# Optimization experiments

Measured on AMD Instinct MI355X. Metric: run time of the kernel, lower is better.

The kernel has to match this reference:

```python
import jax, jax.numpy as jnp
import numpy as np

B, CQ, CKV, H, W = 4, 128, 256, 64, 64
NUM_HEADS = 8
SCALE = (CQ // NUM_HEADS) ** (-0.5)


def setup_inputs() -> dict:
    key = jax.random.key(0)
    ks = jax.random.split(key, 10)
    s = 0.02
    return {
        "x_q": jax.random.normal(ks[0], (B, CQ, H, W), dtype=jnp.float32),
        "x_kv": jax.random.normal(ks[1], (B, CKV, H, W), dtype=jnp.float32),
        "Wq": jax.random.normal(ks[2], (CQ, CQ), dtype=jnp.float32) * s,
        "bq": jnp.zeros((CQ,), dtype=jnp.float32),
        "Wk": jax.random.normal(ks[3], (CQ, CKV), dtype=jnp.float32) * s,
        "bk": jnp.zeros((CQ,), dtype=jnp.float32),
        "Wv": jax.random.normal(ks[4], (CQ, CKV), dtype=jnp.float32) * s,
        "bv": jnp.zeros((CQ,), dtype=jnp.float32),
        "Wo": jax.random.normal(ks[5], (CQ, CQ), dtype=jnp.float32) * s,
        "bo": jnp.zeros((CQ,), dtype=jnp.float32),
    }


def _conv1x1(x, Wm, bv_):
    # 1x1 conv == channel-mixing matmul: [B,C,H,W] x [O,C] -> [B,O,H,W]
    return jnp.einsum('bchw,oc->bohw', x, Wm) + bv_[:, None, None]


def reference(x_q, x_kv, Wq, bq, Wk, bk, Wv, bv, Wo, bo):
    b, c, h, w = x_q.shape
    n = h * w
    Q = _conv1x1(x_q, Wq, bq).reshape(b, c, n)   # [B,C,N]
    K = _conv1x1(x_kv, Wk, bk).reshape(b, c, n)  # [B,C,N]
    V = _conv1x1(x_kv, Wv, bv).reshape(b, c, n)  # [B,C,N]
    # attn = softmax(Q^T K * scale) over keys: [B,N,N]
    attn = jax.nn.softmax(jnp.einsum('bcn,bcm->bnm', Q, K) * SCALE, axis=-1)
    out = jnp.einsum('bnm,bcm->bcn', attn, V).reshape(b, c, h, w)
    out = _conv1x1(out, Wo, bo) + x_q
    return out
```

## Files before the change

### kernel.cpp

```cpp
#include <hip/hip_runtime.h>
#include <hip/hip_bf16.h>

typedef __bf16 bf16x8 __attribute__((ext_vector_type(8)));
typedef float f32x4 __attribute__((ext_vector_type(4)));
typedef float f32x16 __attribute__((ext_vector_type(16)));

#define MFMA16(a, b, c) __builtin_amdgcn_mfma_f32_16x16x32_bf16(a, b, c, 0, 0, 0)
#define MFMA32(a, b, c) __builtin_amdgcn_mfma_f32_32x32x16_bf16(a, b, c, 0, 0, 0)

static constexpr int NSP = 4096;
static constexpr float SCALE_L2E = 0.25f * 1.4426950408889634f;

__device__ __forceinline__ bf16x8 ld_frag(const void* p) {
  int4 v = *(const int4*)p;
  return __builtin_bit_cast(bf16x8, v);
}

__device__ __forceinline__ unsigned pk2(float a, float b) {
  unsigned short x = __builtin_bit_cast(unsigned short, (__bf16)a);
  unsigned short y = __builtin_bit_cast(unsigned short, (__bf16)b);
  return (unsigned)x | ((unsigned)y << 16);
}

__device__ __forceinline__ void load_lds16(const void* g, void* l) {
  __builtin_amdgcn_global_load_lds(
      (const __attribute__((address_space(1))) unsigned*)g,
      (__attribute__((address_space(3))) unsigned*)l, 16, 0, 0);
}

__global__ void k_prep(const float* __restrict__ Wq, const float* __restrict__ bq,
                       const float* __restrict__ Wk, const float* __restrict__ Wv,
                       const float* __restrict__ Wo,
                       __bf16* __restrict__ wqb, __bf16* __restrict__ wkb,
                       __bf16* __restrict__ wvb, __bf16* __restrict__ wob,
                       float* __restrict__ bqs) {
  int i = blockIdx.x * 256 + threadIdx.x;
  if (i < 16384)      wqb[i]          = (__bf16)(Wq[i] * SCALE_L2E);
  else if (i < 49152) wkb[i - 16384]  = (__bf16)Wk[i - 16384];
  else if (i < 81920) wvb[i - 49152]  = (__bf16)Wv[i - 49152];
  else if (i < 98304) wob[i - 81920]  = (__bf16)Wo[i - 81920];
  if (i < 128) bqs[i] = bq[i] * SCALE_L2E;
}

template <bool SWZ>
__device__ __forceinline__ void store_tile_T(char* myt, const f32x4* acc, int g, int r,
                                             __bf16* dst_base) {
#pragma unroll
  for (int oc = 0; oc < 8; ++oc) {
#pragma unroll
    for (int rr = 0; rr < 4; ++rr) {
      int o = oc * 16 + g * 4 + rr;
      int byte = (r << 8) + (o << 1);
      byte ^= (r & 7) << 4;
      *(__bf16*)(myt + byte) = (__bf16)acc[oc][rr];
    }
  }
  int l = g * 16 + r;
#pragma unroll
  for (int p = 0; p < 4; ++p) {
    int u = p * 64 + l, row = u >> 4, seg = u & 15;
    int byte = (row << 8) + (seg << 4);
    if (!SWZ) byte ^= (row & 7) << 4;
    int4 v = *(int4*)(myt + byte);
    *(int4*)(dst_base + row * 128 + seg * 8) = v;
  }
}

__global__ __launch_bounds__(256) void k_proj(const float* __restrict__ xq,
                                              const float* __restrict__ xkv,
                                              const __bf16* __restrict__ wqb,
                                              const __bf16* __restrict__ wkb,
                                              const __bf16* __restrict__ wvb,
                                              const float* __restrict__ bqs,
                                              const float* __restrict__ bk,
                                              const float* __restrict__ bv,
                                              __bf16* __restrict__ Qt,
                                              __bf16* __restrict__ Kt,
                                              __bf16* __restrict__ Vm) {
  const int t = threadIdx.x, w = t >> 6, l = t & 63, r = l & 15, g = l >> 4;
  __shared__ __align__(16) char lds[16384];
  char* myt = lds + (w << 12);

  if (blockIdx.x < 256) {
    const int b = blockIdx.x >> 6;
    const int n0 = (blockIdx.x & 63) << 6;
    const int nl = n0 + (w << 4) + r;
    const float* xb = xq + ((size_t)b << 19);
    bf16x8 bx[4];
#pragma unroll
    for (int cc = 0; cc < 4; ++cc) {
#pragma unroll
      for (int i = 0; i < 8; ++i) {
        int c = cc * 32 + g * 8 + i;
        bx[cc][i] = (__bf16)xb[c * 4096 + nl];
      }
    }
    f32x4 acc[8];
#pragma unroll
    for (int oc = 0; oc < 8; ++oc)
#pragma unroll
      for (int rr = 0; rr < 4; ++rr) acc[oc][rr] = bqs[oc * 16 + g * 4 + rr];
#pragma unroll
    for (int oc = 0; oc < 8; ++oc) {
#pragma unroll
      for (int cc = 0; cc < 4; ++cc) {
        bf16x8 a = ld_frag(wqb + (oc * 16 + r) * 128 + cc * 32 + g * 8);
        acc[oc] = MFMA16(a, bx[cc], acc[oc]);
      }
    }
    store_tile_T<false>(myt, acc, g, r, Qt + ((size_t)(b * NSP + n0 + w * 16)) * 128);
  } else {
    const int bid = blockIdx.x - 256;
    const int b = bid >> 6;
    const int n0 = (bid & 63) << 6;
    const int nl = n0 + (w << 4) + r;
    const float* xb = xkv + ((size_t)b << 20);
    bf16x8 bx[8];
#pragma unroll
    for (int cc = 0; cc < 8; ++cc) {
#pragma unroll
      for (int i = 0; i < 8; ++i) {
        int c = cc * 32 + g * 8 + i;
        bx[cc][i] = (__bf16)xb[(size_t)c * 4096 + nl];
      }
    }
    f32x4 acc[8];
#pragma unroll
    for (int oc = 0; oc < 8; ++oc)
#pragma unroll
      for (int rr = 0; rr < 4; ++rr) acc[oc][rr] = bk[oc * 16 + g * 4 + rr];
#pragma unroll
    for (int oc = 0; oc < 8; ++oc) {
#pragma unroll
      for (int cc = 0; cc < 8; ++cc) {
        bf16x8 a = ld_frag(wkb + (oc * 16 + r) * 256 + cc * 32 + g * 8);
        acc[oc] = MFMA16(a, bx[cc], acc[oc]);
      }
    }
    store_tile_T<true>(myt, acc, g, r, Kt + ((size_t)(b * NSP + n0 + w * 16)) * 128);

    f32x4 av[8];
#pragma unroll
    for (int oc = 0; oc < 8; ++oc)
#pragma unroll
      for (int rr = 0; rr < 4; ++rr) av[oc][rr] = bv[oc * 16 + g * 4 + rr];
#pragma unroll
    for (int oc = 0; oc < 8; ++oc) {
#pragma unroll
      for (int cc = 0; cc < 8; ++cc) {
        bf16x8 a = ld_frag(wvb + (oc * 16 + r) * 256 + cc * 32 + g * 8);
        av[oc] = MFMA16(a, bx[cc], av[oc]);
      }
    }
#pragma unroll
    for (int oc = 0; oc < 8; ++oc) {
#pragma unroll
      for (int rr = 0; rr < 4; ++rr) {
        int o = oc * 16 + g * 4 + rr;
        Vm[((size_t)(b * 128 + o) << 12) + (nl ^ ((o & 7) << 3))] = (__bf16)av[oc][rr];
      }
    }
  }
}

template <int SPLIT>
__global__ __launch_bounds__(256, 2) void k_flash(const __bf16* __restrict__ Qt,
                                                  const __bf16* __restrict__ Kt,
                                                  const __bf16* __restrict__ Vm,
                                                  __bf16* __restrict__ Op,
                                                  float2* __restrict__ Ml) {
  const int bid = blockIdx.x;
  const int combo = bid & (4 * SPLIT - 1), qtile = bid / (4 * SPLIT);
  const int b = combo & 3, ks = combo >> 2;
  const int q0 = qtile << 7;
  const int NK = NSP / SPLIT;
  const int t = threadIdx.x, w = t >> 6, l = t & 63;
  const int q31 = l & 31, hi = l >> 5;
  const int swz = (q31 & 7) << 4;

  __shared__ __align__(16) char kl[2][16384];
  __shared__ __align__(16) char vl[2][16384];

  const __bf16* qp = Qt + ((size_t)(b * NSP + q0 + w * 32 + q31)) * 128;
  bf16x8 qf[8];
#pragma unroll
  for (int cc = 0; cc < 8; ++cc) qf[cc] = ld_frag(qp + cc * 16 + hi * 8);

  f32x16 acc[4];
#pragma unroll
  for (int c = 0; c < 4; ++c)
#pragma unroll
    for (int i = 0; i < 16; ++i) acc[c][i] = 0.f;
  float m = -1e30f, lsum = 0.f;

  const char* kbase = (const char*)(Kt + ((size_t)(b * NSP) + ks * NK) * 128);
  const char* vbase = (const char*)(Vm + (size_t)b * 128 * NSP + ks * NK);

  auto STAGE = [&](int bi, int tt) {
#pragma unroll
    for (int i = 0; i < 4; ++i) {
      int c = i * 4 + w;
      load_lds16(kbase + tt * 16384 + c * 1024 + l * 16, &kl[bi][c * 1024]);
    }
#pragma unroll
    for (int i = 0; i < 4; ++i) {
      int c0 = (i * 4 + w) * 8;
      int ch = c0 + (l >> 3);
      load_lds16(vbase + (size_t)ch * 8192 + tt * 128 + (l & 7) * 16,
                 &vl[bi][c0 * 128]);
    }
  };

  STAGE(0, 0);
  __syncthreads();

  const int nit = NK / 64;
  for (int it = 0; it < nit; ++it) {
    const int cur = it & 1;
    if (it + 1 < nit) STAGE(cur ^ 1, it + 1);

    const char* kt = kl[cur];
    f32x16 s0 = {}, s1 = {};
    __builtin_amdgcn_s_setprio(1);
#pragma unroll
    for (int cc = 0; cc < 8; ++cc) {
      int cb = (cc * 32 + hi * 16);
      int a0 = (q31 << 8) + (cb ^ swz);
      s0 = MFMA32(ld_frag(kt + a0), qf[cc], s0);
      int a1 = ((32 + q31) << 8) + (cb ^ swz);
      s1 = MFMA32(ld_frag(kt + a1), qf[cc], s1);
    }
    __builtin_amdgcn_s_setprio(0);

    float mx = s0[0];
#pragma unroll
    for (int i = 1; i < 16; ++i) mx = fmaxf(mx, s0[i]);
#pragma unroll
    for (int i = 0; i < 16; ++i) mx = fmaxf(mx, s1[i]);
    mx = fmaxf(mx, __shfl_xor(mx, 32));
    if (__any(mx - m > 8.f)) {
      float mn = fmaxf(m, mx);
      float a = exp2f(m - mn);
      m = mn;
      lsum *= a;
#pragma unroll
      for (int c = 0; c < 4; ++c)
#pragma unroll
        for (int i = 0; i < 16; ++i) acc[c][i] *= a;
    }
    float rs = 0.f;
#pragma unroll
    for (int i = 0; i < 16; ++i) {
      s0[i] = exp2f(s0[i] - m);
      rs += s0[i];
    }
#pragma unroll
    for (int i = 0; i < 16; ++i) {
      s1[i] = exp2f(s1[i] - m);
      rs += s1[i];
    }
    rs += __shfl_xor(rs, 32);
    lsum += rs;

    unsigned o0[4][2], o1[4][2], r0[4][2], r1[4][2];
#pragma unroll
    for (int q4 = 0; q4 < 4; ++q4) {
      o0[q4][0] = pk2(s0[4 * q4 + 0], s0[4 * q4 + 1]);
      o0[q4][1] = pk2(s0[4 * q4 + 2], s0[4 * q4 + 3]);
      o1[q4][0] = pk2(s1[4 * q4 + 0], s1[4 * q4 + 1]);
      o1[q4][1] = pk2(s1[4 * q4 + 2], s1[4 * q4 + 3]);
    }
#pragma unroll
    for (int q4 = 0; q4 < 4; ++q4) {
      r0[q4][0] = __shfl_xor(o0[q4][0], 32);
      r0[q4][1] = __shfl_xor(o0[q4][1], 32);
      r1[q4][0] = __shfl_xor(o1[q4][0], 32);
      r1[q4][1] = __shfl_xor(o1[q4][1], 32);
    }

    const char* vt = vl[cur];
    __builtin_amdgcn_s_setprio(1);
#pragma unroll
    for (int kb = 0; kb < 2; ++kb) {
      uint4 f0, f1;
      f0.x = hi ? r0[2 * kb + 1][0] : o0[2 * kb][0];
      f0.y = hi ? r0[2 * kb + 1][1] : o0[2 * kb][1];
      f0.z = hi ? o0[2 * kb + 1][0] : r0[2 * kb][0];
      f0.w = hi ? o0[2 * kb + 1][1] : r0[2 * kb][1];
      f1.x = hi ? r1[2 * kb + 1][0] : o1[2 * kb][0];
      f1.y = hi ? r1[2 * kb + 1][1] : o1[2 * kb][1];
      f1.z = hi ? o1[2 * kb + 1][0] : r1[2 * kb][0];
      f1.w = hi ? o1[2 * kb + 1][1] : r1[2 * kb][1];
      bf16x8 pf0 = __builtin_bit_cast(bf16x8, f0);
      bf16x8 pf1 = __builtin_bit_cast(bf16x8, f1);
#pragma unroll
      for (int cht = 0; cht < 4; ++cht) {
        int rowb = (cht * 32 + q31) << 7;
        int va0 = rowb + ((kb * 32 + hi * 16) ^ swz);
        acc[cht] = MFMA32(ld_frag(vt + va0), pf0, acc[cht]);
        int va1 = rowb + ((64 + kb * 32 + hi * 16) ^ swz);
        acc[cht] = MFMA32(ld_frag(vt + va1), pf1, acc[cht]);
      }
    }
    __builtin_amdgcn_s_setprio(0);
    __syncthreads();
  }

  float inv = 1.f / lsum;
  const size_t orow = (size_t)((ks * 4 + b) * NSP + q0 + w * 32 + q31) * 128;
#pragma unroll
  for (int cht = 0; cht < 4; ++cht) {
#pragma unroll
    for (int qq = 0; qq < 4; ++qq) {
      uint2 v;
      v.x = pk2(acc[cht][4 * qq + 0] * inv, acc[cht][4 * qq + 1] * inv);
      v.y = pk2(acc[cht][4 * qq + 2] * inv, acc[cht][4 * qq + 3] * inv);
      *(uint2*)(Op + orow + cht * 32 + qq * 8 + hi * 4) = v;
    }
  }
  if (hi == 0) {
    Ml[(size_t)(ks * 4 + b) * NSP + q0 + w * 32 + q31] = make_float2(m, lsum);
  }
}

template <int SPLIT>
__global__ __launch_bounds__(256) void k_oproj(const __bf16* __restrict__ Op,
                                               const float2* __restrict__ Ml,
                                               const __bf16* __restrict__ wob,
                                               const float* __restrict__ bo,
                                               const float* __restrict__ xq,
                                               float* __restrict__ out) {
  const int b = blockIdx.x >> 6;
  const int n0 = (blockIdx.x & 63) << 6;
  const int t = threadIdx.x, w = t >> 6, l = t & 63, r = l & 15, g = l >> 4;
  const int nl = n0 + (w << 4) + r;

  float2 e[SPLIT];
  float M = -1e30f;
#pragma unroll
  for (int s = 0; s < SPLIT; ++s) {
    e[s] = Ml[(size_t)(s * 4 + b) * NSP + nl];
    M = fmaxf(M, e[s].x);
  }
  float wk[SPLIT], den = 0.f;
#pragma unroll
  for (int s = 0; s < SPLIT; ++s) {
    wk[s] = exp2f(e[s].x - M);
    den += e[s].y * wk[s];
  }
  float inv = 1.f / den;
#pragma unroll
  for (int s = 0; s < SPLIT; ++s) wk[s] *= inv;

  bf16x8 bfr[4];
#pragma unroll
  for (int cc = 0; cc < 4; ++cc) {
    float a8[8];
#pragma unroll
    for (int j = 0; j < 8; ++j) a8[j] = 0.f;
#pragma unroll
    for (int s = 0; s < SPLIT; ++s) {
      bf16x8 a = ld_frag(Op + ((size_t)(s * 4 + b) * NSP + nl) * 128 + cc * 32 + g * 8);
#pragma unroll
      for (int j = 0; j < 8; ++j) a8[j] += (float)a[j] * wk[s];
    }
#pragma unroll
    for (int j = 0; j < 8; ++j) bfr[cc][j] = (__bf16)a8[j];
  }

  f32x4 acc[8];
#pragma unroll
  for (int oc = 0; oc < 8; ++oc)
#pragma unroll
    for (int rr = 0; rr < 4; ++rr) acc[oc][rr] = bo[oc * 16 + g * 4 + rr];
#pragma unroll
  for (int oc = 0; oc < 8; ++oc) {
#pragma unroll
    for (int cc = 0; cc < 4; ++cc) {
      bf16x8 a = ld_frag(wob + (oc * 16 + r) * 128 + cc * 32 + g * 8);
      acc[oc] = MFMA16(a, bfr[cc], acc[oc]);
    }
  }
#pragma unroll
  for (int oc = 0; oc < 8; ++oc) {
#pragma unroll
    for (int rr = 0; rr < 4; ++rr) {
      int o = oc * 16 + g * 4 + rr;
      size_t idx = ((size_t)(b * 128 + o) << 12) + nl;
      out[idx] = acc[oc][rr] + xq[idx];
    }
  }
}

extern "C" void kernel_launch(void* const* d_in, const int* in_sizes, int n_in,
                              void* d_out, int out_size, void* d_ws, size_t ws_size,
                              hipStream_t stream) {
  const float* xq = (const float*)d_in[0];
  const float* xkv = (const float*)d_in[1];
  const float* Wq = (const float*)d_in[2];
  const float* bq = (const float*)d_in[3];
  const float* Wk = (const float*)d_in[4];
  const float* bk = (const float*)d_in[5];
  const float* Wv = (const float*)d_in[6];
  const float* bv = (const float*)d_in[7];
  const float* Wo = (const float*)d_in[8];
  const float* bo = (const float*)d_in[9];
  float* out = (float*)d_out;

  char* ws = (char*)d_ws;
  __bf16* wqb = (__bf16*)(ws);
  __bf16* wkb = (__bf16*)(ws + 32768);
  __bf16* wvb = (__bf16*)(ws + 98304);
  __bf16* wob = (__bf16*)(ws + 163840);
  float* bqs = (float*)(ws + 196608);
  __bf16* Qt = (__bf16*)(ws + 197120);
  __bf16* Kt = (__bf16*)(ws + 197120 + 4194304);
  __bf16* Vm = (__bf16*)(ws + 197120 + 2 * 4194304);
  __bf16* Op = (__bf16*)(ws + 197120 + 3 * 4194304);
  float2* Ml = (float2*)(ws + 197120 + 3 * 4194304 + 16777216);

  k_prep<<<dim3(384), dim3(256), 0, stream>>>(Wq, bq, Wk, Wv, Wo, wqb, wkb, wvb, wob, bqs);
  k_proj<<<dim3(512), dim3(256), 0, stream>>>(xq, xkv, wqb, wkb, wvb, bqs, bk, bv,
                                              Qt, Kt, Vm);

  const size_t need4 = 197120ull + 3ull * 4194304 + 16777216 + 524288;
  if (ws_size >= need4) {
    k_flash<4><<<dim3(512), dim3(256), 0, stream>>>(Qt, Kt, Vm, Op, Ml);
    k_oproj<4><<<dim3(256), dim3(256), 0, stream>>>(Op, Ml, wob, bo, xq, out);
  } else {
    k_flash<2><<<dim3(256), dim3(256), 0, stream>>>(Qt, Kt, Vm, Op, Ml);
    k_oproj<2><<<dim3(256), dim3(256), 0, stream>>>(Op, Ml, wob, bo, xq, out);
  }
}
```

Baseline: 97.17 us.

## Process two query subtiles per wave sharing K/V fragments, smaller KV tiles, split 8

```diff
diff --git a/kernel.cpp b/kernel.cpp
--- a/kernel.cpp
+++ b/kernel.cpp
@@ -157,7 +157,7 @@
 #pragma unroll
       for (int rr = 0; rr < 4; ++rr) {
         int o = oc * 16 + g * 4 + rr;
-        Vm[((size_t)(b * 128 + o) << 12) + (nl ^ ((o & 7) << 3))] = (__bf16)av[oc][rr];
+        Vm[((size_t)(b * 128 + o) << 12) + (nl ^ ((o & 3) << 3))] = (__bf16)av[oc][rr];
       }
     }
   }
@@ -172,154 +172,158 @@
   const int bid = blockIdx.x;
   const int combo = bid & (4 * SPLIT - 1), qtile = bid / (4 * SPLIT);
   const int b = combo & 3, ks = combo >> 2;
-  const int q0 = qtile << 7;
+  const int q0 = qtile << 8;
   const int NK = NSP / SPLIT;
   const int t = threadIdx.x, w = t >> 6, l = t & 63;
   const int q31 = l & 31, hi = l >> 5;
   const int swz = (q31 & 7) << 4;
-
-  __shared__ __align__(16) char kl[2][16384];
-  __shared__ __align__(16) char vl[2][16384];
-
-  const __bf16* qp = Qt + ((size_t)(b * NSP + q0 + w * 32 + q31)) * 128;
-  bf16x8 qf[8];
-#pragma unroll
-  for (int cc = 0; cc < 8; ++cc) qf[cc] = ld_frag(qp + cc * 16 + hi * 8);
-
-  f32x16 acc[4];
-#pragma unroll
-  for (int c = 0; c < 4; ++c)
-#pragma unroll
-    for (int i = 0; i < 16; ++i) acc[c][i] = 0.f;
-  float m = -1e30f, lsum = 0.f;
+  const int swzV = (q31 & 3) << 4;
+
+  __shared__ __align__(16) char kl[2][8192];
+  __shared__ __align__(16) char vl[2][8192];
+
+  const int qA = q0 + w * 64 + q31;
+  const __bf16* qpA = Qt + ((size_t)(b * NSP + qA)) * 128;
+  bf16x8 qfA[8], qfB[8];
+#pragma unroll
+  for (int cc = 0; cc < 8; ++cc) {
+    qfA[cc] = ld_frag(qpA + cc * 16 + hi * 8);
+    qfB[cc] = ld_frag(qpA + 32 * 128 + cc * 16 + hi * 8);
+  }
+
+  f32x16 accA[4], accB[4];
+#pragma unroll
+  for (int c = 0; c < 4; ++c) {
+#pragma unroll
+    for (int i = 0; i < 16; ++i) { accA[c][i] = 0.f; accB[c][i] = 0.f; }
+  }
+  float mA = -1e30f, lA = 0.f, mB = -1e30f, lB = 0.f;
 
   const char* kbase = (const char*)(Kt + ((size_t)(b * NSP) + ks * NK) * 128);
   const char* vbase = (const char*)(Vm + (size_t)b * 128 * NSP + ks * NK);
 
   auto STAGE = [&](int bi, int tt) {
 #pragma unroll
-    for (int i = 0; i < 4; ++i) {
-      int c = i * 4 + w;
-      load_lds16(kbase + tt * 16384 + c * 1024 + l * 16, &kl[bi][c * 1024]);
-    }
-#pragma unroll
-    for (int i = 0; i < 4; ++i) {
-      int c0 = (i * 4 + w) * 8;
-      int ch = c0 + (l >> 3);
-      load_lds16(vbase + (size_t)ch * 8192 + tt * 128 + (l & 7) * 16,
-                 &vl[bi][c0 * 128]);
+    for (int i = 0; i < 2; ++i) {
+      int u = i * 256 + t;
+      load_lds16(kbase + tt * 8192 + u * 16, &kl[bi][u * 16]);
+    }
+#pragma unroll
+    for (int i = 0; i < 2; ++i) {
+      int u = i * 256 + t, ch = u >> 2, ko = u & 3;
+      load_lds16(vbase + (size_t)ch * 8192 + tt * 64 + ko * 16, &vl[bi][u * 16]);
     }
   };
 
   STAGE(0, 0);
   __syncthreads();
 
-  const int nit = NK / 64;
+  const int nit = NK / 32;
   for (int it = 0; it < nit; ++it) {
     const int cur = it & 1;
     if (it + 1 < nit) STAGE(cur ^ 1, it + 1);
 
     const char* kt = kl[cur];
-    f32x16 s0 = {}, s1 = {};
+    f32x16 sA = {}, sB = {};
     __builtin_amdgcn_s_setprio(1);
 #pragma unroll
     for (int cc = 0; cc < 8; ++cc) {
-      int cb = (cc * 32 + hi * 16);
-      int a0 = (q31 << 8) + (cb ^ swz);
-      s0 = MFMA32(ld_frag(kt + a0), qf[cc], s0);
-      int a1 = ((32 + q31) << 8) + (cb ^ swz);
-      s1 = MFMA32(ld_frag(kt + a1), qf[cc], s1);
+      bf16x8 kf = ld_frag(kt + (q31 << 8) + ((cc * 32 + hi * 16) ^ swz));
+      sA = MFMA32(kf, qfA[cc], sA);
+      sB = MFMA32(kf, qfB[cc], sB);
     }
     __builtin_amdgcn_s_setprio(0);
 
-    float mx = s0[0];
-#pragma unroll
-    for (int i = 1; i < 16; ++i) mx = fmaxf(mx, s0[i]);
-#pragma unroll
-    for (int i = 0; i < 16; ++i) mx = fmaxf(mx, s1[i]);
-    mx = fmaxf(mx, __shfl_xor(mx, 32));
-    if (__any(mx - m > 8.f)) {
-      float mn = fmaxf(m, mx);
-      float a = exp2f(m - mn);
-      m = mn;
-      lsum *= a;
-#pragma unroll
-      for (int c = 0; c < 4; ++c)
-#pragma unroll
-        for (int i = 0; i < 16; ++i) acc[c][i] *= a;
-    }
-    float rs = 0.f;
+    float mxA = sA[0], mxB = sB[0];
+#pragma unroll
+    for (int i = 1; i < 16; ++i) { mxA = fmaxf(mxA, sA[i]); mxB = fmaxf(mxB, sB[i]); }
+    mxA = fmaxf(mxA, __shfl_xor(mxA, 32));
+    mxB = fmaxf(mxB, __shfl_xor(mxB, 32));
+    if (__any(fmaxf(mxA - mA, mxB - mB) > 8.f)) {
+      float nA = fmaxf(mA, mxA), nB = fmaxf(mB, mxB);
+      float aA = exp2f(mA - nA), aB = exp2f(mB - nB);
+      mA = nA; mB = nB;
+      lA *= aA; lB *= aB;
+#pragma unroll
+      for (int c = 0; c < 4; ++c) {
+#pragma unroll
+        for (int i = 0; i < 16; ++i) { accA[c][i] *= aA; accB[c][i] *= aB; }
+      }
+    }
+    float rsA = 0.f, rsB = 0.f;
 #pragma unroll
     for (int i = 0; i < 16; ++i) {
-      s0[i] = exp2f(s0[i] - m);
-      rs += s0[i];
-    }
-#pragma unroll
-    for (int i = 0; i < 16; ++i) {
-      s1[i] = exp2f(s1[i] - m);
-      rs += s1[i];
-    }
-    rs += __shfl_xor(rs, 32);
-    lsum += rs;
-
-    unsigned o0[4][2], o1[4][2], r0[4][2], r1[4][2];
+      sA[i] = exp2f(sA[i] - mA);
+      sB[i] = exp2f(sB[i] - mB);
+      rsA += sA[i];
+      rsB += sB[i];
+    }
+    rsA += __shfl_xor(rsA, 32);
+    rsB += __shfl_xor(rsB, 32);
+    lA += rsA;
+    lB += rsB;
+
+    unsigned pA[4][2], pB[4][2], rA[4][2], rB[4][2];
 #pragma unroll
     for (int q4 = 0; q4 < 4; ++q4) {
-      o0[q4][0] = pk2(s0[4 * q4 + 0], s0[4 * q4 + 1]);
-      o0[q4][1] = pk2(s0[4 * q4 + 2], s0[4 * q4 + 3]);
-      o1[q4][0] = pk2(s1[4 * q4 + 0], s1[4 * q4 + 1]);
-      o1[q4][1] = pk2(s1[4 * q4 + 2], s1[4 * q4 + 3]);
+      pA[q4][0] = pk2(sA[4 * q4 + 0], sA[4 * q4 + 1]);
+      pA[q4][1] = pk2(sA[4 * q4 + 2], sA[4 * q4 + 3]);
+      pB[q4][0] = pk2(sB[4 * q4 + 0], sB[4 * q4 + 1]);
+      pB[q4][1] = pk2(sB[4 * q4 + 2], sB[4 * q4 + 3]);
     }
 #pragma unroll
     for (int q4 = 0; q4 < 4; ++q4) {
-      r0[q4][0] = __shfl_xor(o0[q4][0], 32);
-      r0[q4][1] = __shfl_xor(o0[q4][1], 32);
-      r1[q4][0] = __shfl_xor(o1[q4][0], 32);
-      r1[q4][1] = __shfl_xor(o1[q4][1], 32);
+      rA[q4][0] = __shfl_xor(pA[q4][0], 32);
+      rA[q4][1] = __shfl_xor(pA[q4][1], 32);
+      rB[q4][0] = __shfl_xor(pB[q4][0], 32);
+      rB[q4][1] = __shfl_xor(pB[q4][1], 32);
     }
 
     const char* vt = vl[cur];
     __builtin_amdgcn_s_setprio(1);
 #pragma unroll
     for (int kb = 0; kb < 2; ++kb) {
-      uint4 f0, f1;
-      f0.x = hi ? r0[2 * kb + 1][0] : o0[2 * kb][0];
-      f0.y = hi ? r0[2 * kb + 1][1] : o0[2 * kb][1];
-      f0.z = hi ? o0[2 * kb + 1][0] : r0[2 * kb][0];
-      f0.w = hi ? o0[2 * kb + 1][1] : r0[2 * kb][1];
-      f1.x = hi ? r1[2 * kb + 1][0] : o1[2 * kb][0];
-      f1.y = hi ? r1[2 * kb + 1][1] : o1[2 * kb][1];
-      f1.z = hi ? o1[2 * kb + 1][0] : r1[2 * kb][0];
-      f1.w = hi ? o1[2 * kb + 1][1] : r1[2 * kb][1];
-      bf16x8 pf0 = __builtin_bit_cast(bf16x8, f0);
-      bf16x8 pf1 = __builtin_bit_cast(bf16x8, f1);
+      uint4 fa, fb;
+      fa.x = hi ? rA[2 * kb + 1][0] : pA[2 * kb][0];
+      fa.y = hi ? rA[2 * kb + 1][1] : pA[2 * kb][1];
+      fa.z = hi ? pA[2 * kb + 1][0] : rA[2 * kb][0];
+      fa.w = hi ? pA[2 * kb + 1][1] : rA[2 * kb][1];
+      fb.x = hi ? rB[2 * kb + 1][0] : pB[2 * kb][0];
+      fb.y = hi ? rB[2 * kb + 1][1] : pB[2 * kb][1];
+      fb.z = hi ? pB[2 * kb + 1][0] : rB[2 * kb][0];
+      fb.w = hi ? pB[2 * kb + 1][1] : rB[2 * kb][1];
+      bf16x8 pfA = __builtin_bit_cast(bf16x8, fa);
+      bf16x8 pfB = __builtin_bit_cast(bf16x8, fb);
 #pragma unroll
       for (int cht = 0; cht < 4; ++cht) {
-        int rowb = (cht * 32 + q31) << 7;
-        int va0 = rowb + ((kb * 32 + hi * 16) ^ swz);
-        acc[cht] = MFMA32(ld_frag(vt + va0), pf0, acc[cht]);
-        int va1 = rowb + ((64 + kb * 32 + hi * 16) ^ swz);
-        acc[cht] = MFMA32(ld_frag(vt + va1), pf1, acc[cht]);
+        bf16x8 vf = ld_frag(vt + (cht * 32 + q31) * 64 + ((kb * 32 + hi * 16) ^ swzV));
+        accA[cht] = MFMA32(vf, pfA, accA[cht]);
+        accB[cht] = MFMA32(vf, pfB, accB[cht]);
       }
     }
     __builtin_amdgcn_s_setprio(0);
     __syncthreads();
   }
 
-  float inv = 1.f / lsum;
-  const size_t orow = (size_t)((ks * 4 + b) * NSP + q0 + w * 32 + q31) * 128;
+  float invA = 1.f / lA, invB = 1.f / lB;
+  const size_t rowA = (size_t)((ks * 4 + b) * NSP + qA) * 128;
 #pragma unroll
   for (int cht = 0; cht < 4; ++cht) {
 #pragma unroll
     for (int qq = 0; qq < 4; ++qq) {
-      uint2 v;
-      v.x = pk2(acc[cht][4 * qq + 0] * inv, acc[cht][4 * qq + 1] * inv);
-      v.y = pk2(acc[cht][4 * qq + 2] * inv, acc[cht][4 * qq + 3] * inv);
-      *(uint2*)(Op + orow + cht * 32 + qq * 8 + hi * 4) = v;
+      uint2 va, vb;
+      va.x = pk2(accA[cht][4 * qq + 0] * invA, accA[cht][4 * qq + 1] * invA);
+      va.y = pk2(accA[cht][4 * qq + 2] * invA, accA[cht][4 * qq + 3] * invA);
+      vb.x = pk2(accB[cht][4 * qq + 0] * invB, accB[cht][4 * qq + 1] * invB);
+      vb.y = pk2(accB[cht][4 * qq + 2] * invB, accB[cht][4 * qq + 3] * invB);
+      *(uint2*)(Op + rowA + cht * 32 + qq * 8 + hi * 4) = va;
+      *(uint2*)(Op + rowA + 32 * 128 + cht * 32 + qq * 8 + hi * 4) = vb;
     }
   }
   if (hi == 0) {
-    Ml[(size_t)(ks * 4 + b) * NSP + q0 + w * 32 + q31] = make_float2(m, lsum);
+    size_t mlrow = (size_t)(ks * 4 + b) * NSP + qA;
+    Ml[mlrow] = make_float2(mA, lA);
+    Ml[mlrow + 32] = make_float2(mB, lB);
   }
 }
 
@@ -417,18 +421,25 @@
   __bf16* Kt = (__bf16*)(ws + 197120 + 4194304);
   __bf16* Vm = (__bf16*)(ws + 197120 + 2 * 4194304);
   __bf16* Op = (__bf16*)(ws + 197120 + 3 * 4194304);
-  float2* Ml = (float2*)(ws + 197120 + 3 * 4194304 + 16777216);
+  float2* Ml = (float2*)(ws + 197120 + 3 * 4194304 + 33554432);
 
   k_prep<<<dim3(384), dim3(256), 0, stream>>>(Wq, bq, Wk, Wv, Wo, wqb, wkb, wvb, wob, bqs);
   k_proj<<<dim3(512), dim3(256), 0, stream>>>(xq, xkv, wqb, wkb, wvb, bqs, bk, bv,
                                               Qt, Kt, Vm);
 
-  const size_t need4 = 197120ull + 3ull * 4194304 + 16777216 + 524288;
-  if (ws_size >= need4) {
-    k_flash<4><<<dim3(512), dim3(256), 0, stream>>>(Qt, Kt, Vm, Op, Ml);
-    k_oproj<4><<<dim3(256), dim3(256), 0, stream>>>(Op, Ml, wob, bo, xq, out);
+  const size_t base = 197120ull + 3ull * 4194304;
+  const size_t need8 = base + 33554432ull + 1048576ull;
+  const size_t need4 = base + 16777216ull + 524288ull;
+  if (ws_size >= need8) {
+    k_flash<8><<<dim3(512), dim3(256), 0, stream>>>(Qt, Kt, Vm, Op, Ml);
+    k_oproj<8><<<dim3(256), dim3(256), 0, stream>>>(Op, Ml, wob, bo, xq, out);
+  } else if (ws_size >= need4) {
+    float2* Ml4 = (float2*)(ws + base + 16777216);
+    k_flash<4><<<dim3(256), dim3(256), 0, stream>>>(Qt, Kt, Vm, Op, Ml4);
+    k_oproj<4><<<dim3(256), dim3(256), 0, stream>>>(Op, Ml4, wob, bo, xq, out);
   } else {
-    k_flash<2><<<dim3(256), dim3(256), 0, stream>>>(Qt, Kt, Vm, Op, Ml);
-    k_oproj<2><<<dim3(256), dim3(256), 0, stream>>>(Op, Ml, wob, bo, xq, out);
-  }
-}
+    float2* Ml2 = (float2*)(ws + base + 8388608);
+    k_flash<2><<<dim3(128), dim3(256), 0, stream>>>(Qt, Kt, Vm, Op, Ml2);
+    k_oproj<2><<<dim3(256), dim3(256), 0, stream>>>(Op, Ml2, wob, bo, xq, out);
+  }
+}
```

Result: slower. 101.1 us (+4.1%).
